# Kernel tuning notes

Hardware: AMD Instinct MI355X
Metric: run time of the kernel (lower is better)

## Reference

```python
import jax, jax.numpy as jnp
import numpy as np

N = 20000
E = 320000
IN_CH = 512
OUT_CH = 256


def setup_inputs() -> dict:
    key = jax.random.key(0)
    ks = jax.random.split(key, 24)
    p = lambda k, shape: jax.random.normal(k, shape, jnp.float32) * 0.05
    return {
        "x": jax.random.normal(ks[0], (N, IN_CH), jnp.float32),
        "edge_index": jax.random.randint(ks[1], (2, E), 0, N),
        "original_size": 16384,
        "W1": p(ks[2], (IN_CH, 4 * 256)), "as1": p(ks[3], (4, 256)), "ad1": p(ks[4], (4, 256)), "b1": p(ks[5], (1024,)),
        "lw1": p(ks[6], (IN_CH, 1024)), "lb1": p(ks[7], (1024,)),
        "W2": p(ks[8], (1024, 4 * 256)), "as2": p(ks[9], (4, 256)), "ad2": p(ks[10], (4, 256)), "b2": p(ks[11], (1024,)),
        "lw2": p(ks[12], (1024, 1024)), "lb2": p(ks[13], (1024,)),
        "W3": p(ks[14], (1024, 6 * 256)), "as3": p(ks[15], (6, 256)), "ad3": p(ks[16], (6, 256)), "b3": p(ks[17], (256,)),
        "lw3": p(ks[18], (1024, OUT_CH)), "lb3": p(ks[19], (OUT_CH,)),
    }


def gat_conv(x, src, dst, W, a_src, a_dst, bias, heads, ch, concat):
    """PyG-style GATConv: gather -> edge attention -> segment softmax -> scatter-add."""
    n = x.shape[0]
    h = (x @ W).reshape(n, heads, ch)                      # [N,H,C]
    alpha_s = (h * a_src[None]).sum(-1)                    # [N,H]
    alpha_d = (h * a_dst[None]).sum(-1)                    # [N,H]
    e = jax.nn.leaky_relu(alpha_s[src] + alpha_d[dst], 0.2)  # [E,H]
    m = jax.ops.segment_max(e, dst, num_segments=n)        # per-dst max (stable softmax)
    e = jnp.exp(e - m[dst])
    denom = jax.ops.segment_sum(e, dst, num_segments=n)
    alpha = e / (denom[dst] + 1e-16)                       # [E,H]
    msg = h[src] * alpha[:, :, None]                       # [E,H,C]
    out = jax.ops.segment_sum(msg, dst, num_segments=n)    # [N,H,C]
    out = out.reshape(n, heads * ch) if concat else out.mean(axis=1)
    return out + bias


def reference(x, edge_index, original_size, W1, as1, ad1, b1, lw1, lb1,
              W2, as2, ad2, b2, lw2, lb2, W3, as3, ad3, b3, lw3, lb3):
    n = x.shape[0]
    loops = jnp.arange(n)
    src = jnp.concatenate([edge_index[0], loops])  # PyG add_self_loops=True default
    dst = jnp.concatenate([edge_index[1], loops])
    h = jax.nn.elu(gat_conv(x, src, dst, W1, as1, ad1, b1, 4, 256, True) + x @ lw1 + lb1)
    h = jax.nn.elu(gat_conv(h, src, dst, W2, as2, ad2, b2, 4, 256, True) + h @ lw2 + lb2)
    h = gat_conv(h, src, dst, W3, as3, ad3, b3, 6, 256, False) + h @ lw3 + lb3
    return h[:original_size]
```

## Files before the change

### kernel.cpp

```cpp
#include <hip/hip_runtime.h>

#define N_NODES 20000
#define M_PAD   20096
#define E_EDGES 320000

typedef unsigned short u16;
typedef unsigned int   u32;
typedef __attribute__((ext_vector_type(8))) short bf16x8;
typedef __attribute__((ext_vector_type(4))) float f32x4;
typedef __attribute__((ext_vector_type(4))) u32   u32x4;

__device__ __forceinline__ float bf2f(u16 u){
  u32 x = ((u32)u) << 16; float f; __builtin_memcpy(&f, &x, 4); return f;
}
__device__ __forceinline__ u16 f2bf(float f){
  u32 u; __builtin_memcpy(&u, &f, 4);
  u += 0x7fffu + ((u >> 16) & 1u);
  return (u16)(u >> 16);
}

__device__ __forceinline__ void gl_lds16(const void* g, void* l){
  __builtin_amdgcn_global_load_lds((const __attribute__((address_space(1))) void*)g,
                                   (__attribute__((address_space(3))) void*)l, 16, 0, 0);
}

__device__ __forceinline__ void acc8(float* acc, float w, u32x4 p){
#pragma unroll
  for (int d = 0; d < 4; d++){
    u32 u = p[d];
    acc[2 * d]     += w * bf2f((u16)(u & 0xffff));
    acc[2 * d + 1] += w * bf2f((u16)(u >> 16));
  }
}

__global__ void hist_k(const int* __restrict__ ei, int* __restrict__ cnt){
  int i = blockIdx.x * 256 + threadIdx.x;
  if (i < E_EDGES) atomicAdd(&cnt[ei[E_EDGES + i]], 1);
}

__global__ void scan_k(const int* __restrict__ cnt, int* __restrict__ rowp,
                       int* __restrict__ fill, int n){
  __shared__ int wsum[16], wpre[16];
  __shared__ int carry;
  int tid = threadIdx.x, lane = tid & 63, wv = tid >> 6;
  if (tid == 0) carry = 0;
  __syncthreads();
  for (int base = 0; base < n; base += 1024){
    int i = base + tid;
    int v = (i < n) ? cnt[i] : 0;
    int incl = v;
#pragma unroll
    for (int d = 1; d < 64; d <<= 1){
      int t = __shfl_up(incl, d, 64);
      if (lane >= d) incl += t;
    }
    if (lane == 63) wsum[wv] = incl;
    __syncthreads();
    if (tid == 0){
      int s = carry;
#pragma unroll
      for (int w = 0; w < 16; w++){ wpre[w] = s; s += wsum[w]; }
      carry = s;
    }
    __syncthreads();
    if (i < n){ int e = wpre[wv] + incl - v; rowp[i] = e; fill[i] = e; }
  }
  __syncthreads();
  if (tid == 0) rowp[n] = carry;
}

__global__ void scatter_k(const int* __restrict__ ei, int* __restrict__ fill, int* __restrict__ esrc){
  int i = blockIdx.x * 256 + threadIdx.x;
  if (i < E_EDGES){
    int d = ei[E_EDGES + i];
    int p = atomicAdd(&fill[d], 1);
    esrc[p] = ei[i];
  }
}

__global__ void tcast_all(const float* __restrict__ W1, const float* __restrict__ lw1, u16* __restrict__ Wt1,
                          const float* __restrict__ W2, const float* __restrict__ lw2, u16* __restrict__ Wt2,
                          const float* __restrict__ W3, const float* __restrict__ lw3, u16* __restrict__ Wt3)
{
  __shared__ float tile[32][33];
  int b = blockIdx.x;
  const float* src; u16* dst; int Nc, n0, ldd;
  if      (b <  512){            src = W1;  Nc = 1024; dst = Wt1; n0 = 0;    ldd = 512;  }
  else if (b < 1024){ b -=  512; src = lw1; Nc = 1024; dst = Wt1; n0 = 1024; ldd = 512;  }
  else if (b < 2048){ b -= 1024; src = W2;  Nc = 1024; dst = Wt2; n0 = 0;    ldd = 1024; }
  else if (b < 3072){ b -= 2048; src = lw2; Nc = 1024; dst = Wt2; n0 = 1024; ldd = 1024; }
  else if (b < 4608){ b -= 3072; src = W3;  Nc = 1536; dst = Wt3; n0 = 0;    ldd = 1024; }
  else              { b -= 4608; src = lw3; Nc = 256;  dst = Wt3; n0 = 1536; ldd = 1024; }
  int gx = Nc / 32;
  int kb = (b / gx) * 32, nb = (b % gx) * 32;
  int tx = threadIdx.x, ty = threadIdx.y;
#pragma unroll
  for (int r = 0; r < 32; r += 8)
    tile[ty + r][tx] = src[(size_t)(kb + ty + r) * Nc + nb + tx];
  __syncthreads();
#pragma unroll
  for (int r = 0; r < 32; r += 8){
    int n = nb + ty + r;
    dst[(size_t)(n0 + n) * ldd + kb + tx] = f2bf(tile[tx][ty + r]);
  }
}

__global__ void castx_k(const float* __restrict__ x, u16* __restrict__ o, int realRows){
  int r = blockIdx.x, c = threadIdx.x * 2;
  float2 v = (r < realRows) ? *(const float2*)(x + (size_t)r * 512 + c) : make_float2(0.f, 0.f);
  u32 pk = ((u32)f2bf(v.y) << 16) | (u32)f2bf(v.x);
  *(u32*)(o + (size_t)r * 512 + c) = pk;
}

__global__ void zpad_k(u16* __restrict__ p, int n){
  int i = blockIdx.x * 256 + threadIdx.x; if (i < n) p[i] = 0;
}

__global__ __launch_bounds__(256, 2)
void gemm_bf16(const u16* __restrict__ A, const u16* __restrict__ Bt, u16* __restrict__ C,
               int N, int K,
               const float* __restrict__ a_s, const float* __restrict__ a_d,
               float* __restrict__ aS, float* __restrict__ aD, int H)
{
  __shared__ __attribute__((aligned(16))) u16 lA[128 * 32];
  __shared__ __attribute__((aligned(16))) u16 lB[256 * 32];
  const int tid  = threadIdx.x;
  const int wave = tid >> 6, lane = tid & 63;
  const int bn = blockIdx.x, bm = blockIdx.y;
  const int wm = (wave >> 1) * 64, wn = (wave & 1) * 128;

  const int srow  = wave * 16 + (lane >> 2);
  const int skcol = (lane & 3) * 8;
  const u16* Ag0 = A  + (size_t)(bm * 128 + srow) * K + skcol;
  const u16* Ag1 = Ag0 + (size_t)64 * K;
  const u16* Bg  = Bt + (size_t)(bn * 256 + srow) * K + skcol;
  u16* lA0 = lA + wave * 512; u16* lA1 = lA + 2048 + wave * 512;
  u16* lBw = lB + wave * 512;

  f32x4 acc[4][8] = {};

  for (int k0 = 0; k0 < K; k0 += 32){
    gl_lds16(Ag0 + k0, lA0);
    gl_lds16(Ag1 + k0, lA1);
#pragma unroll
    for (int c = 0; c < 4; c++)
      gl_lds16(Bg + (size_t)(c * 64) * K + k0, lBw + c * 2048);
    __syncthreads();
    const int koff = (lane >> 4) * 8;
    const int rsel = lane & 15;
    bf16x8 af[4], bfr[8];
#pragma unroll
    for (int i = 0; i < 4; i++) af[i]  = *(const bf16x8*)&lA[(wm + i * 16 + rsel) * 32 + koff];
#pragma unroll
    for (int j = 0; j < 8; j++) bfr[j] = *(const bf16x8*)&lB[(wn + j * 16 + rsel) * 32 + koff];
#pragma unroll
    for (int i = 0; i < 4; i++)
#pragma unroll
      for (int j = 0; j < 8; j++)
        acc[i][j] = __builtin_amdgcn_mfma_f32_16x16x32_bf16(af[i], bfr[j], acc[i][j], 0, 0, 0);
    __syncthreads();
  }

  const int r0 = (lane >> 4) * 4, cl = lane & 15;
#pragma unroll
  for (int i = 0; i < 4; i++)
#pragma unroll
    for (int j = 0; j < 8; j++){
      int row = bm * 128 + wm + i * 16 + r0;
      int col = bn * 256 + wn + j * 16 + cl;
      u16* cp = C + (size_t)row * N + col;
#pragma unroll
      for (int r = 0; r < 4; r++) cp[(size_t)r * N] = f2bf(acc[i][j][r]);
    }

  if (bn < H){
    float* fa = (float*)lA;
    fa[tid]       = a_s[bn * 256 + tid];
    fa[256 + tid] = a_d[bn * 256 + tid];
    __syncthreads();
    float* fb = (float*)lB;
    const int q = lane >> 4;
#pragma unroll
    for (int i = 0; i < 4; i++)
#pragma unroll
      for (int r = 0; r < 4; r++){
        float ps = 0.f, pd = 0.f;
#pragma unroll
        for (int j = 0; j < 8; j++){
          float v = acc[i][j][r];
          int c = wn + j * 16 + cl;
          ps += v * fa[c];
          pd += v * fa[256 + c];
        }
#pragma unroll
        for (int m = 1; m < 16; m <<= 1){
          ps += __shfl_xor(ps, m, 64);
          pd += __shfl_xor(pd, m, 64);
        }
        if (cl == 0){
          int row = wm + i * 16 + q * 4 + r;
          fb[(wave & 1) * 128 + row]       = ps;
          fb[256 + (wave & 1) * 128 + row] = pd;
        }
      }
    __syncthreads();
    if (tid < 128){
      int row = bm * 128 + tid;
      aS[(size_t)row * H + bn] = fb[tid] + fb[128 + tid];
      aD[(size_t)row * H + bn] = fb[256 + tid] + fb[384 + tid];
    }
  }
}

__global__ __launch_bounds__(256)
void agg4_k(const u16* __restrict__ HG, int ldH,
            const int* __restrict__ rowp, const int* __restrict__ esrc,
            const float* __restrict__ aS, const float* __restrict__ aD,
            const float* __restrict__ bias, const float* __restrict__ lbias,
            u16* __restrict__ outb)
{
  constexpr int MAXE = 320;
  __shared__ float s_m[4], s_dinv[4], s_red[16];
  __shared__ float s_ew[MAXE * 4];
  __shared__ int   s_src[MAXE];
  __shared__ float s_acc[2][1024];

  const int dst = blockIdx.x;
  const int tid = threadIdx.x, lane = tid & 63, wv = tid >> 6;
  const int e0 = rowp[dst];
  const int deg = rowp[dst + 1] - e0;
  const int nE = deg + 1;
  const bool fits = (nE <= MAXE);

  float4 adv = *(const float4*)(aD + (size_t)dst * 4);

  float lm[4] = { -1e30f, -1e30f, -1e30f, -1e30f };
  for (int i = tid; i < nE; i += 256){
    int s = (i == deg) ? dst : esrc[e0 + i];
    if (fits) s_src[i] = s;
    float4 as = *(const float4*)(aS + (size_t)s * 4);
    float e0h = as.x + adv.x; e0h = e0h > 0.f ? e0h : 0.2f * e0h;
    float e1h = as.y + adv.y; e1h = e1h > 0.f ? e1h : 0.2f * e1h;
    float e2h = as.z + adv.z; e2h = e2h > 0.f ? e2h : 0.2f * e2h;
    float e3h = as.w + adv.w; e3h = e3h > 0.f ? e3h : 0.2f * e3h;
    if (fits){ s_ew[i*4+0]=e0h; s_ew[i*4+1]=e1h; s_ew[i*4+2]=e2h; s_ew[i*4+3]=e3h; }
    lm[0] = fmaxf(lm[0], e0h); lm[1] = fmaxf(lm[1], e1h);
    lm[2] = fmaxf(lm[2], e2h); lm[3] = fmaxf(lm[3], e3h);
  }
#pragma unroll
  for (int h = 0; h < 4; h++)
#pragma unroll
    for (int off = 32; off; off >>= 1) lm[h] = fmaxf(lm[h], __shfl_down(lm[h], off));
  if (lane == 0){
#pragma unroll
    for (int h = 0; h < 4; h++) s_red[wv * 4 + h] = lm[h];
  }
  __syncthreads();
  if (tid < 4) s_m[tid] = fmaxf(fmaxf(s_red[tid], s_red[4 + tid]),
                                fmaxf(s_red[8 + tid], s_red[12 + tid]));
  __syncthreads();

  float ls[4] = {0.f, 0.f, 0.f, 0.f};
  for (int i = tid; i < nE; i += 256){
    if (fits){
#pragma unroll
      for (int h = 0; h < 4; h++){
        float w = __expf(s_ew[i * 4 + h] - s_m[h]);
        s_ew[i * 4 + h] = w;
        ls[h] += w;
      }
    } else {
      int s = (i == deg) ? dst : esrc[e0 + i];
      float4 as = *(const float4*)(aS + (size_t)s * 4);
      float e;
      e = as.x + adv.x; e = e > 0.f ? e : 0.2f * e; ls[0] += __expf(e - s_m[0]);
      e = as.y + adv.y; e = e > 0.f ? e : 0.2f * e; ls[1] += __expf(e - s_m[1]);
      e = as.z + adv.z; e = e > 0.f ? e : 0.2f * e; ls[2] += __expf(e - s_m[2]);
      e = as.w + adv.w; e = e > 0.f ? e : 0.2f * e; ls[3] += __expf(e - s_m[3]);
    }
  }
#pragma unroll
  for (int h = 0; h < 4; h++)
#pragma unroll
    for (int off = 32; off; off >>= 1) ls[h] += __shfl_down(ls[h], off);
  if (lane == 0){
#pragma unroll
    for (int h = 0; h < 4; h++) s_red[wv * 4 + h] = ls[h];
  }
  __syncthreads();
  if (tid < 4) s_dinv[tid] = 1.f / (s_red[tid] + s_red[4 + tid] + s_red[8 + tid] + s_red[12 + tid] + 1e-16f);
  __syncthreads();

  const int grp = wv >> 1;
  const int ch0 = (wv & 1) * 512 + lane * 8;
  const int h   = ch0 >> 8;
  const float dinv = s_dinv[h];
  const float mh   = s_m[h];
  float acc[8] = {};
  const u16* HGb = HG + ch0;

  if (fits){
    int i = grp;
    for (; i + 2 < nE; i += 4){
      int s0 = s_src[i], s1 = s_src[i + 2];
      float w0 = s_ew[i * 4 + h] * dinv;
      float w1 = s_ew[(i + 2) * 4 + h] * dinv;
      u32x4 p0 = *(const u32x4*)(HGb + (size_t)s0 * ldH);
      u32x4 p1 = *(const u32x4*)(HGb + (size_t)s1 * ldH);
      acc8(acc, w0, p0);
      acc8(acc, w1, p1);
    }
    if (i < nE){
      int s0 = s_src[i];
      float w0 = s_ew[i * 4 + h] * dinv;
      u32x4 p0 = *(const u32x4*)(HGb + (size_t)s0 * ldH);
      acc8(acc, w0, p0);
    }
  } else {
    float advh = aD[(size_t)dst * 4 + h];
    for (int i = grp; i < nE; i += 2){
      int s = (i == deg) ? dst : esrc[e0 + i];
      float e = aS[(size_t)s * 4 + h] + advh;
      e = e > 0.f ? e : 0.2f * e;
      float w = __expf(e - mh) * dinv;
      u32x4 p = *(const u32x4*)(HGb + (size_t)s * ldH);
      acc8(acc, w, p);
    }
  }
#pragma unroll
  for (int c = 0; c < 8; c++) s_acc[grp][ch0 + c] = acc[c];
  __syncthreads();

  const int c4 = tid * 4;
  const u16* lr = HG + (size_t)dst * ldH + 1024 + c4;
  ushort4 u = *(const ushort4*)lr;
  float lv[4] = { bf2f(u.x), bf2f(u.y), bf2f(u.z), bf2f(u.w) };
  ushort4 o;
  float v0 = s_acc[0][c4+0] + s_acc[1][c4+0] + bias[c4+0] + lv[0] + lbias[c4+0]; v0 = v0 > 0.f ? v0 : __expf(v0) - 1.f;
  float v1 = s_acc[0][c4+1] + s_acc[1][c4+1] + bias[c4+1] + lv[1] + lbias[c4+1]; v1 = v1 > 0.f ? v1 : __expf(v1) - 1.f;
  float v2 = s_acc[0][c4+2] + s_acc[1][c4+2] + bias[c4+2] + lv[2] + lbias[c4+2]; v2 = v2 > 0.f ? v2 : __expf(v2) - 1.f;
  float v3 = s_acc[0][c4+3] + s_acc[1][c4+3] + bias[c4+3] + lv[3] + lbias[c4+3]; v3 = v3 > 0.f ? v3 : __expf(v3) - 1.f;
  o.x = f2bf(v0); o.y = f2bf(v1); o.z = f2bf(v2); o.w = f2bf(v3);
  *(ushort4*)(outb + (size_t)dst * 1024 + c4) = o;
}

__global__ __launch_bounds__(384)
void agg6_k(const u16* __restrict__ HG, int ldH,
            const int* __restrict__ rowp, const int* __restrict__ esrc,
            const float* __restrict__ aS, const float* __restrict__ aD,
            const float* __restrict__ bias, const float* __restrict__ lbias,
            float* __restrict__ outf)
{
  constexpr int MAXE = 320;
  __shared__ float s_m[6], s_dinv[6], s_red[36];
  __shared__ float s_ew[MAXE * 6];
  __shared__ int   s_src[MAXE];
  __shared__ float s_acc[2][1536];

  const int dst = blockIdx.x;
  const int tid = threadIdx.x, lane = tid & 63, wv = tid >> 6;
  const int e0 = rowp[dst];
  const int deg = rowp[dst + 1] - e0;
  const int nE = deg + 1;
  const bool fits = (nE <= MAXE);

  float adv[6];
#pragma unroll
  for (int h = 0; h < 6; h++) adv[h] = aD[(size_t)dst * 6 + h];

  float lm[6];
#pragma unroll
  for (int h = 0; h < 6; h++) lm[h] = -1e30f;
  for (int i = tid; i < nE; i += 384){
    int s = (i == deg) ? dst : esrc[e0 + i];
    if (fits) s_src[i] = s;
#pragma unroll
    for (int h = 0; h < 6; h++){
      float e = aS[(size_t)s * 6 + h] + adv[h];
      e = e > 0.f ? e : 0.2f * e;
      if (fits) s_ew[i * 6 + h] = e;
      lm[h] = fmaxf(lm[h], e);
    }
  }
#pragma unroll
  for (int h = 0; h < 6; h++)
#pragma unroll
    for (int off = 32; off; off >>= 1) lm[h] = fmaxf(lm[h], __shfl_down(lm[h], off));
  if (lane == 0){
#pragma unroll
    for (int h = 0; h < 6; h++) s_red[wv * 6 + h] = lm[h];
  }
  __syncthreads();
  if (tid < 6){
    float m = s_red[tid];
#pragma unroll
    for (int w = 1; w < 6; w++) m = fmaxf(m, s_red[w * 6 + tid]);
    s_m[tid] = m;
  }
  __syncthreads();

  float ls[6];
#pragma unroll
  for (int h = 0; h < 6; h++) ls[h] = 0.f;
  for (int i = tid; i < nE; i += 384){
    if (fits){
#pragma unroll
      for (int h = 0; h < 6; h++){
        float w = __expf(s_ew[i * 6 + h] - s_m[h]);
        s_ew[i * 6 + h] = w;
        ls[h] += w;
      }
    } else {
      int s = (i == deg) ? dst : esrc[e0 + i];
#pragma unroll
      for (int h = 0; h < 6; h++){
        float e = aS[(size_t)s * 6 + h] + adv[h];
        e = e > 0.f ? e : 0.2f * e;
        ls[h] += __expf(e - s_m[h]);
      }
    }
  }
#pragma unroll
  for (int h = 0; h < 6; h++)
#pragma unroll
    for (int off = 32; off; off >>= 1) ls[h] += __shfl_down(ls[h], off);
  if (lane == 0){
#pragma unroll
    for (int h = 0; h < 6; h++) s_red[wv * 6 + h] = ls[h];
  }
  __syncthreads();
  if (tid < 6){
    float s = 0.f;
#pragma unroll
    for (int w = 0; w < 6; w++) s += s_red[w * 6 + tid];
    s_dinv[tid] = 1.f / (s + 1e-16f);
  }
  __syncthreads();

  const int grp  = wv / 3;
  const int wrow = wv - grp * 3;
  const int ch0  = wrow * 512 + lane * 8;
  const int h    = ch0 >> 8;
  const float dinv = s_dinv[h];
  const float mh   = s_m[h];
  float acc[8] = {};
  const u16* HGb = HG + ch0;

  if (fits){
    int i = grp;
    for (; i + 2 < nE; i += 4){
      int s0 = s_src[i], s1 = s_src[i + 2];
      float w0 = s_ew[i * 6 + h] * dinv;
      float w1 = s_ew[(i + 2) * 6 + h] * dinv;
      u32x4 p0 = *(const u32x4*)(HGb + (size_t)s0 * ldH);
      u32x4 p1 = *(const u32x4*)(HGb + (size_t)s1 * ldH);
      acc8(acc, w0, p0);
      acc8(acc, w1, p1);
    }
    if (i < nE){
      int s0 = s_src[i];
      float w0 = s_ew[i * 6 + h] * dinv;
      u32x4 p0 = *(const u32x4*)(HGb + (size_t)s0 * ldH);
      acc8(acc, w0, p0);
    }
  } else {
    float advh = aD[(size_t)dst * 6 + h];
    for (int i = grp; i < nE; i += 2){
      int s = (i == deg) ? dst : esrc[e0 + i];
      float e = aS[(size_t)s * 6 + h] + advh;
      e = e > 0.f ? e : 0.2f * e;
      float w = __expf(e - mh) * dinv;
      u32x4 p = *(const u32x4*)(HGb + (size_t)s * ldH);
      acc8(acc, w, p);
    }
  }
#pragma unroll
  for (int c = 0; c < 8; c++) s_acc[grp][ch0 + c] = acc[c];
  __syncthreads();

  if (tid < 256){
    int c = tid;
    float v = 0.f;
#pragma unroll
    for (int hh = 0; hh < 6; hh++) v += s_acc[0][hh * 256 + c] + s_acc[1][hh * 256 + c];
    v = v * (1.f / 6.f) + bias[c] + bf2f(HG[(size_t)dst * ldH + 1536 + c]) + lbias[c];
    outf[(size_t)dst * 256 + c] = v;
  }
}

extern "C" void kernel_launch(void* const* d_in, const int* in_sizes, int n_in,
                              void* d_out, int out_size, void* d_ws, size_t ws_size,
                              hipStream_t stream)
{
  const float* x   = (const float*)d_in[0];
  const int*   ei  = (const int*)  d_in[1];
  const float* W1  = (const float*)d_in[3];
  const float* as1 = (const float*)d_in[4];
  const float* ad1 = (const float*)d_in[5];
  const float* b1  = (const float*)d_in[6];
  const float* lw1 = (const float*)d_in[7];
  const float* lb1 = (const float*)d_in[8];
  const float* W2  = (const float*)d_in[9];
  const float* as2 = (const float*)d_in[10];
  const float* ad2 = (const float*)d_in[11];
  const float* b2  = (const float*)d_in[12];
  const float* lw2 = (const float*)d_in[13];
  const float* lb2 = (const float*)d_in[14];
  const float* W3  = (const float*)d_in[15];
  const float* as3 = (const float*)d_in[16];
  const float* ad3 = (const float*)d_in[17];
  const float* b3  = (const float*)d_in[18];
  const float* lw3 = (const float*)d_in[19];
  const float* lb3 = (const float*)d_in[20];

  char* wp = (char*)d_ws;
  auto nxt = [&](size_t b) -> void* {
    void* p = (void*)wp; wp += (b + 255) & ~(size_t)255; return p;
  };
  u16*  Wt1  = (u16*) nxt((size_t)2048 * 512  * 2);
  u16*  Wt2  = (u16*) nxt((size_t)2048 * 1024 * 2);
  u16*  Wt3  = (u16*) nxt((size_t)1792 * 1024 * 2);
  u16*  Xb   = (u16*) nxt((size_t)M_PAD * 1024 * 2);
  u16*  HG   = (u16*) nxt((size_t)M_PAD * 2048 * 2);
  float* aS  = (float*)nxt((size_t)M_PAD * 6 * 4);
  float* aD  = (float*)nxt((size_t)M_PAD * 6 * 4);
  int*  cnt  = (int*)  nxt((size_t)N_NODES * 4);
  int*  rowp = (int*)  nxt((size_t)(N_NODES + 1) * 4);
  int*  fill = (int*)  nxt((size_t)N_NODES * 4);
  int*  esrc = (int*)  nxt((size_t)E_EDGES * 4);

  hipMemsetAsync(cnt, 0, (size_t)N_NODES * 4, stream);
  hist_k   <<<(E_EDGES + 255) / 256, 256, 0, stream>>>(ei, cnt);
  scan_k   <<<1, 1024, 0, stream>>>(cnt, rowp, fill, N_NODES);
  scatter_k<<<(E_EDGES + 255) / 256, 256, 0, stream>>>(ei, fill, esrc);

  tcast_all<<<4864, dim3(32, 8), 0, stream>>>(W1, lw1, Wt1, W2, lw2, Wt2, W3, lw3, Wt3);

  castx_k<<<M_PAD, 256, 0, stream>>>(x, Xb, N_NODES);
  zpad_k <<<(96 * 1024 + 255) / 256, 256, 0, stream>>>(Xb + (size_t)N_NODES * 1024, 96 * 1024);

  const int MT = M_PAD / 128;

  gemm_bf16<<<dim3(2048 / 256, MT), 256, 0, stream>>>(Xb, Wt1, HG, 2048, 512,  as1, ad1, aS, aD, 4);
  agg4_k   <<<N_NODES, 256, 0, stream>>>(HG, 2048, rowp, esrc, aS, aD, b1, lb1, Xb);

  gemm_bf16<<<dim3(2048 / 256, MT), 256, 0, stream>>>(Xb, Wt2, HG, 2048, 1024, as2, ad2, aS, aD, 4);
  agg4_k   <<<N_NODES, 256, 0, stream>>>(HG, 2048, rowp, esrc, aS, aD, b2, lb2, Xb);

  gemm_bf16<<<dim3(1792 / 256, MT), 256, 0, stream>>>(Xb, Wt3, HG, 1792, 1024, as3, ad3, aS, aD, 6);
  int outRows = out_size / 256;
  agg6_k   <<<outRows, 384, 0, stream>>>(HG, 1792, rowp, esrc, aS, aD, b3, lb3, (float*)d_out);

  (void)in_sizes; (void)n_in; (void)ws_size;
}
```

Before: 873.7 us.

## Aggregate one destination node per wavefront instead of one per block

The GAT aggregation kernels now give each 64-lane wavefront a whole destination node, four nodes per block. Softmax max and sum use wave shuffles instead of block-wide shared-memory reductions and several barriers. Each lane holds one edge's source and weight, so the first 64 edges are broadcast by shuffle, and each lane accumulates 16 or 24 channels. The per-node attention-score arrays are padded to a stride of 8 so they can be read with vector loads. Degrees above 64 fall back to a serial loop that recomputes the weights, and the launch grid assumes the node count divides by 4.

After: 865.2 us. Within noise of the previous version (-1.0%).

```diff
diff --git a/kernel.cpp b/kernel.cpp
--- a/kernel.cpp
+++ b/kernel.cpp
@@ -18,6 +18,7 @@
   u += 0x7fffu + ((u >> 16) & 1u);
   return (u16)(u >> 16);
 }
+__device__ __forceinline__ float lrelu(float x){ return x > 0.f ? x : 0.2f * x; }
 
 __device__ __forceinline__ void gl_lds16(const void* g, void* l){
   __builtin_amdgcn_global_load_lds((const __attribute__((address_space(1))) void*)g,
@@ -31,6 +32,25 @@
     acc[2 * d]     += w * bf2f((u16)(u & 0xffff));
     acc[2 * d + 1] += w * bf2f((u16)(u >> 16));
   }
+}
+
+__device__ __forceinline__ void acc24(float* acc, float w0, float w1, int bnd,
+                                      u32x4 p0, u32x4 p1, u32x4 p2){
+  u32 u[12];
+  *(u32x4*)(u) = p0; *(u32x4*)(u + 4) = p1; *(u32x4*)(u + 8) = p2;
+#pragma unroll
+  for (int d = 0; d < 12; d++){
+    float w = (2 * d < bnd) ? w0 : w1;
+    acc[2 * d]     += w * bf2f((u16)(u[d] & 0xffff));
+    acc[2 * d + 1] += w * bf2f((u16)(u[d] >> 16));
+  }
+}
+
+__device__ __forceinline__ float sel6(const float* a, int h){
+  float r = a[0];
+  r = (h == 1) ? a[1] : r; r = (h == 2) ? a[2] : r; r = (h == 3) ? a[3] : r;
+  r = (h == 4) ? a[4] : r; r = (h == 5) ? a[5] : r;
+  return r;
 }
 
 __global__ void hist_k(const int* __restrict__ ei, int* __restrict__ cnt){
@@ -206,286 +226,238 @@
     __syncthreads();
     if (tid < 128){
       int row = bm * 128 + tid;
-      aS[(size_t)row * H + bn] = fb[tid] + fb[128 + tid];
-      aD[(size_t)row * H + bn] = fb[256 + tid] + fb[384 + tid];
+      aS[(size_t)row * 8 + bn] = fb[tid] + fb[128 + tid];
+      aD[(size_t)row * 8 + bn] = fb[256 + tid] + fb[384 + tid];
     }
   }
 }
 
 __global__ __launch_bounds__(256)
-void agg4_k(const u16* __restrict__ HG, int ldH,
-            const int* __restrict__ rowp, const int* __restrict__ esrc,
-            const float* __restrict__ aS, const float* __restrict__ aD,
-            const float* __restrict__ bias, const float* __restrict__ lbias,
-            u16* __restrict__ outb)
+void agg4w_k(const u16* __restrict__ HG, int ldH,
+             const int* __restrict__ rowp, const int* __restrict__ esrc,
+             const float* __restrict__ aS, const float* __restrict__ aD,
+             const float* __restrict__ bias, const float* __restrict__ lbias,
+             u16* __restrict__ outb)
 {
-  constexpr int MAXE = 320;
-  __shared__ float s_m[4], s_dinv[4], s_red[16];
-  __shared__ float s_ew[MAXE * 4];
-  __shared__ int   s_src[MAXE];
-  __shared__ float s_acc[2][1024];
-
-  const int dst = blockIdx.x;
+  __shared__ float s_w[4][256];
   const int tid = threadIdx.x, lane = tid & 63, wv = tid >> 6;
+  const int dst = blockIdx.x * 4 + wv;
   const int e0 = rowp[dst];
   const int deg = rowp[dst + 1] - e0;
   const int nE = deg + 1;
-  const bool fits = (nE <= MAXE);
-
-  float4 adv = *(const float4*)(aD + (size_t)dst * 4);
-
-  float lm[4] = { -1e30f, -1e30f, -1e30f, -1e30f };
-  for (int i = tid; i < nE; i += 256){
+  const float4 adv = *(const float4*)(aD + (size_t)dst * 8);
+
+  int myS = dst;
+  float ea = -1e30f, eb = -1e30f, ec = -1e30f, ed = -1e30f;
+  if (lane < nE){
+    myS = (lane == deg) ? dst : esrc[e0 + lane];
+    float4 as = *(const float4*)(aS + (size_t)myS * 8);
+    ea = lrelu(as.x + adv.x); eb = lrelu(as.y + adv.y);
+    ec = lrelu(as.z + adv.z); ed = lrelu(as.w + adv.w);
+  }
+  float m0 = ea, m1 = eb, m2 = ec, m3 = ed;
+  for (int i = lane + 64; i < nE; i += 64){
     int s = (i == deg) ? dst : esrc[e0 + i];
-    if (fits) s_src[i] = s;
-    float4 as = *(const float4*)(aS + (size_t)s * 4);
-    float e0h = as.x + adv.x; e0h = e0h > 0.f ? e0h : 0.2f * e0h;
-    float e1h = as.y + adv.y; e1h = e1h > 0.f ? e1h : 0.2f * e1h;
-    float e2h = as.z + adv.z; e2h = e2h > 0.f ? e2h : 0.2f * e2h;
-    float e3h = as.w + adv.w; e3h = e3h > 0.f ? e3h : 0.2f * e3h;
-    if (fits){ s_ew[i*4+0]=e0h; s_ew[i*4+1]=e1h; s_ew[i*4+2]=e2h; s_ew[i*4+3]=e3h; }
-    lm[0] = fmaxf(lm[0], e0h); lm[1] = fmaxf(lm[1], e1h);
-    lm[2] = fmaxf(lm[2], e2h); lm[3] = fmaxf(lm[3], e3h);
-  }
-#pragma unroll
-  for (int h = 0; h < 4; h++)
-#pragma unroll
-    for (int off = 32; off; off >>= 1) lm[h] = fmaxf(lm[h], __shfl_down(lm[h], off));
-  if (lane == 0){
-#pragma unroll
-    for (int h = 0; h < 4; h++) s_red[wv * 4 + h] = lm[h];
-  }
+    float4 as = *(const float4*)(aS + (size_t)s * 8);
+    m0 = fmaxf(m0, lrelu(as.x + adv.x)); m1 = fmaxf(m1, lrelu(as.y + adv.y));
+    m2 = fmaxf(m2, lrelu(as.z + adv.z)); m3 = fmaxf(m3, lrelu(as.w + adv.w));
+  }
+#pragma unroll
+  for (int off = 1; off < 64; off <<= 1){
+    m0 = fmaxf(m0, __shfl_xor(m0, off)); m1 = fmaxf(m1, __shfl_xor(m1, off));
+    m2 = fmaxf(m2, __shfl_xor(m2, off)); m3 = fmaxf(m3, __shfl_xor(m3, off));
+  }
+
+  float w0 = __expf(ea - m0), w1 = __expf(eb - m1);
+  float w2 = __expf(ec - m2), w3 = __expf(ed - m3);
+  float l0 = w0, l1 = w1, l2 = w2, l3 = w3;
+  for (int i = lane + 64; i < nE; i += 64){
+    int s = (i == deg) ? dst : esrc[e0 + i];
+    float4 as = *(const float4*)(aS + (size_t)s * 8);
+    l0 += __expf(lrelu(as.x + adv.x) - m0); l1 += __expf(lrelu(as.y + adv.y) - m1);
+    l2 += __expf(lrelu(as.z + adv.z) - m2); l3 += __expf(lrelu(as.w + adv.w) - m3);
+  }
+#pragma unroll
+  for (int off = 1; off < 64; off <<= 1){
+    l0 += __shfl_xor(l0, off); l1 += __shfl_xor(l1, off);
+    l2 += __shfl_xor(l2, off); l3 += __shfl_xor(l3, off);
+  }
+  float d0 = 1.f / (l0 + 1e-16f), d1 = 1.f / (l1 + 1e-16f);
+  float d2 = 1.f / (l2 + 1e-16f), d3 = 1.f / (l3 + 1e-16f);
+  *(float4*)&s_w[wv][lane * 4] = make_float4(w0 * d0, w1 * d1, w2 * d2, w3 * d3);
   __syncthreads();
-  if (tid < 4) s_m[tid] = fmaxf(fmaxf(s_red[tid], s_red[4 + tid]),
-                                fmaxf(s_red[8 + tid], s_red[12 + tid]));
-  __syncthreads();
-
-  float ls[4] = {0.f, 0.f, 0.f, 0.f};
-  for (int i = tid; i < nE; i += 256){
-    if (fits){
-#pragma unroll
-      for (int h = 0; h < 4; h++){
-        float w = __expf(s_ew[i * 4 + h] - s_m[h]);
-        s_ew[i * 4 + h] = w;
-        ls[h] += w;
-      }
-    } else {
-      int s = (i == deg) ? dst : esrc[e0 + i];
-      float4 as = *(const float4*)(aS + (size_t)s * 4);
-      float e;
-      e = as.x + adv.x; e = e > 0.f ? e : 0.2f * e; ls[0] += __expf(e - s_m[0]);
-      e = as.y + adv.y; e = e > 0.f ? e : 0.2f * e; ls[1] += __expf(e - s_m[1]);
-      e = as.z + adv.z; e = e > 0.f ? e : 0.2f * e; ls[2] += __expf(e - s_m[2]);
-      e = as.w + adv.w; e = e > 0.f ? e : 0.2f * e; ls[3] += __expf(e - s_m[3]);
-    }
-  }
-#pragma unroll
-  for (int h = 0; h < 4; h++)
-#pragma unroll
-    for (int off = 32; off; off >>= 1) ls[h] += __shfl_down(ls[h], off);
-  if (lane == 0){
-#pragma unroll
-    for (int h = 0; h < 4; h++) s_red[wv * 4 + h] = ls[h];
-  }
-  __syncthreads();
-  if (tid < 4) s_dinv[tid] = 1.f / (s_red[tid] + s_red[4 + tid] + s_red[8 + tid] + s_red[12 + tid] + 1e-16f);
-  __syncthreads();
-
-  const int grp = wv >> 1;
-  const int ch0 = (wv & 1) * 512 + lane * 8;
-  const int h   = ch0 >> 8;
-  const float dinv = s_dinv[h];
-  const float mh   = s_m[h];
-  float acc[8] = {};
-  const u16* HGb = HG + ch0;
-
-  if (fits){
-    int i = grp;
-    for (; i + 2 < nE; i += 4){
-      int s0 = s_src[i], s1 = s_src[i + 2];
-      float w0 = s_ew[i * 4 + h] * dinv;
-      float w1 = s_ew[(i + 2) * 4 + h] * dinv;
-      u32x4 p0 = *(const u32x4*)(HGb + (size_t)s0 * ldH);
-      u32x4 p1 = *(const u32x4*)(HGb + (size_t)s1 * ldH);
-      acc8(acc, w0, p0);
-      acc8(acc, w1, p1);
-    }
-    if (i < nE){
-      int s0 = s_src[i];
-      float w0 = s_ew[i * 4 + h] * dinv;
-      u32x4 p0 = *(const u32x4*)(HGb + (size_t)s0 * ldH);
-      acc8(acc, w0, p0);
-    }
-  } else {
-    float advh = aD[(size_t)dst * 4 + h];
-    for (int i = grp; i < nE; i += 2){
-      int s = (i == deg) ? dst : esrc[e0 + i];
-      float e = aS[(size_t)s * 4 + h] + advh;
-      e = e > 0.f ? e : 0.2f * e;
-      float w = __expf(e - mh) * dinv;
-      u32x4 p = *(const u32x4*)(HGb + (size_t)s * ldH);
-      acc8(acc, w, p);
-    }
-  }
-#pragma unroll
-  for (int c = 0; c < 8; c++) s_acc[grp][ch0 + c] = acc[c];
-  __syncthreads();
-
-  const int c4 = tid * 4;
-  const u16* lr = HG + (size_t)dst * ldH + 1024 + c4;
-  ushort4 u = *(const ushort4*)lr;
-  float lv[4] = { bf2f(u.x), bf2f(u.y), bf2f(u.z), bf2f(u.w) };
-  ushort4 o;
-  float v0 = s_acc[0][c4+0] + s_acc[1][c4+0] + bias[c4+0] + lv[0] + lbias[c4+0]; v0 = v0 > 0.f ? v0 : __expf(v0) - 1.f;
-  float v1 = s_acc[0][c4+1] + s_acc[1][c4+1] + bias[c4+1] + lv[1] + lbias[c4+1]; v1 = v1 > 0.f ? v1 : __expf(v1) - 1.f;
-  float v2 = s_acc[0][c4+2] + s_acc[1][c4+2] + bias[c4+2] + lv[2] + lbias[c4+2]; v2 = v2 > 0.f ? v2 : __expf(v2) - 1.f;
-  float v3 = s_acc[0][c4+3] + s_acc[1][c4+3] + bias[c4+3] + lv[3] + lbias[c4+3]; v3 = v3 > 0.f ? v3 : __expf(v3) - 1.f;
-  o.x = f2bf(v0); o.y = f2bf(v1); o.z = f2bf(v2); o.w = f2bf(v3);
-  *(ushort4*)(outb + (size_t)dst * 1024 + c4) = o;
-}
-
-__global__ __launch_bounds__(384)
-void agg6_k(const u16* __restrict__ HG, int ldH,
-            const int* __restrict__ rowp, const int* __restrict__ esrc,
-            const float* __restrict__ aS, const float* __restrict__ aD,
-            const float* __restrict__ bias, const float* __restrict__ lbias,
-            float* __restrict__ outf)
+
+  const int h = lane >> 4;
+  const int ch0 = lane * 16;
+  const float mh   = (h < 2) ? (h == 0 ? m0 : m1) : (h == 2 ? m2 : m3);
+  const float dh   = (h < 2) ? (h == 0 ? d0 : d1) : (h == 2 ? d2 : d3);
+  const float advh = (h < 2) ? (h == 0 ? adv.x : adv.y) : (h == 2 ? adv.z : adv.w);
+  float acc[16] = {};
+  const u16* HGc = HG + ch0;
+  const int nF = nE < 64 ? nE : 64;
+  int i = 0;
+  for (; i + 1 < nF; i += 2){
+    int sA = __shfl(myS, i), sB = __shfl(myS, i + 1);
+    float wA = s_w[wv][i * 4 + h], wB = s_w[wv][(i + 1) * 4 + h];
+    const u16* ra = HGc + (size_t)sA * ldH;
+    const u16* rb = HGc + (size_t)sB * ldH;
+    u32x4 pa0 = *(const u32x4*)ra, pa1 = *(const u32x4*)(ra + 8);
+    u32x4 pb0 = *(const u32x4*)rb, pb1 = *(const u32x4*)(rb + 8);
+    acc8(acc, wA, pa0); acc8(acc + 8, wA, pa1);
+    acc8(acc, wB, pb0); acc8(acc + 8, wB, pb1);
+  }
+  if (i < nF){
+    int sA = __shfl(myS, i);
+    float wA = s_w[wv][i * 4 + h];
+    const u16* ra = HGc + (size_t)sA * ldH;
+    acc8(acc, wA, *(const u32x4*)ra); acc8(acc + 8, wA, *(const u32x4*)(ra + 8));
+  }
+  for (int j = 64; j < nE; j++){
+    int s = (j == deg) ? dst : esrc[e0 + j];
+    float e = lrelu(aS[(size_t)s * 8 + h] + advh);
+    float w = __expf(e - mh) * dh;
+    const u16* r = HGc + (size_t)s * ldH;
+    acc8(acc, w, *(const u32x4*)r); acc8(acc + 8, w, *(const u32x4*)(r + 8));
+  }
+
+  const u16* lr = HG + (size_t)dst * ldH + 1024 + ch0;
+  u32x4 q0 = *(const u32x4*)lr, q1 = *(const u32x4*)(lr + 8);
+  float lin[16];
+#pragma unroll
+  for (int d = 0; d < 4; d++){
+    lin[2*d]     = bf2f((u16)(q0[d] & 0xffff)); lin[2*d+1]   = bf2f((u16)(q0[d] >> 16));
+    lin[8+2*d]   = bf2f((u16)(q1[d] & 0xffff)); lin[8+2*d+1] = bf2f((u16)(q1[d] >> 16));
+  }
+  u32 o[8];
+#pragma unroll
+  for (int d = 0; d < 8; d++){
+    float va = acc[2*d]   + bias[ch0 + 2*d]   + lin[2*d]   + lbias[ch0 + 2*d];
+    float vb = acc[2*d+1] + bias[ch0 + 2*d+1] + lin[2*d+1] + lbias[ch0 + 2*d+1];
+    va = va > 0.f ? va : __expf(va) - 1.f;
+    vb = vb > 0.f ? vb : __expf(vb) - 1.f;
+    o[d] = ((u32)f2bf(vb) << 16) | (u32)f2bf(va);
+  }
+  u16* op = outb + (size_t)dst * 1024 + ch0;
+  *(u32x4*)op = *(u32x4*)o;
+  *(u32x4*)(op + 8) = *(u32x4*)(o + 4);
+}
+
+__global__ __launch_bounds__(256)
+void agg6w_k(const u16* __restrict__ HG, int ldH,
+             const int* __restrict__ rowp, const int* __restrict__ esrc,
+             const float* __restrict__ aS, const float* __restrict__ aD,
+             const float* __restrict__ bias, const float* __restrict__ lbias,
+             float* __restrict__ outf)
 {
-  constexpr int MAXE = 320;
-  __shared__ float s_m[6], s_dinv[6], s_red[36];
-  __shared__ float s_ew[MAXE * 6];
-  __shared__ int   s_src[MAXE];
-  __shared__ float s_acc[2][1536];
-
-  const int dst = blockIdx.x;
+  __shared__ float s_w[4][64 * 6];
+  __shared__ float s_fin[4][1536];
   const int tid = threadIdx.x, lane = tid & 63, wv = tid >> 6;
+  const int dst = blockIdx.x * 4 + wv;
   const int e0 = rowp[dst];
   const int deg = rowp[dst + 1] - e0;
   const int nE = deg + 1;
-  const bool fits = (nE <= MAXE);
-
-  float adv[6];
-#pragma unroll
-  for (int h = 0; h < 6; h++) adv[h] = aD[(size_t)dst * 6 + h];
-
-  float lm[6];
-#pragma unroll
-  for (int h = 0; h < 6; h++) lm[h] = -1e30f;
-  for (int i = tid; i < nE; i += 384){
+
+  const float* advp = aD + (size_t)dst * 8;
+  float4 av4 = *(const float4*)advp; float2 av2 = *(const float2*)(advp + 4);
+  float adv[6] = { av4.x, av4.y, av4.z, av4.w, av2.x, av2.y };
+
+  int myS = dst;
+  float e[6];
+#pragma unroll
+  for (int h = 0; h < 6; h++) e[h] = -1e30f;
+  if (lane < nE){
+    myS = (lane == deg) ? dst : esrc[e0 + lane];
+    float4 a0 = *(const float4*)(aS + (size_t)myS * 8);
+    float2 a1 = *(const float2*)(aS + (size_t)myS * 8 + 4);
+    e[0] = lrelu(a0.x + adv[0]); e[1] = lrelu(a0.y + adv[1]);
+    e[2] = lrelu(a0.z + adv[2]); e[3] = lrelu(a0.w + adv[3]);
+    e[4] = lrelu(a1.x + adv[4]); e[5] = lrelu(a1.y + adv[5]);
+  }
+  float m[6];
+#pragma unroll
+  for (int h = 0; h < 6; h++) m[h] = e[h];
+  for (int i = lane + 64; i < nE; i += 64){
     int s = (i == deg) ? dst : esrc[e0 + i];
-    if (fits) s_src[i] = s;
-#pragma unroll
-    for (int h = 0; h < 6; h++){
-      float e = aS[(size_t)s * 6 + h] + adv[h];
-      e = e > 0.f ? e : 0.2f * e;
-      if (fits) s_ew[i * 6 + h] = e;
-      lm[h] = fmaxf(lm[h], e);
-    }
+    float4 a0 = *(const float4*)(aS + (size_t)s * 8);
+    float2 a1 = *(const float2*)(aS + (size_t)s * 8 + 4);
+    float t[6] = { a0.x, a0.y, a0.z, a0.w, a1.x, a1.y };
+#pragma unroll
+    for (int h = 0; h < 6; h++) m[h] = fmaxf(m[h], lrelu(t[h] + adv[h]));
   }
 #pragma unroll
   for (int h = 0; h < 6; h++)
 #pragma unroll
-    for (int off = 32; off; off >>= 1) lm[h] = fmaxf(lm[h], __shfl_down(lm[h], off));
-  if (lane == 0){
-#pragma unroll
-    for (int h = 0; h < 6; h++) s_red[wv * 6 + h] = lm[h];
-  }
+    for (int off = 1; off < 64; off <<= 1) m[h] = fmaxf(m[h], __shfl_xor(m[h], off));
+
+  float w[6], l[6];
+#pragma unroll
+  for (int h = 0; h < 6; h++){ w[h] = __expf(e[h] - m[h]); l[h] = w[h]; }
+  for (int i = lane + 64; i < nE; i += 64){
+    int s = (i == deg) ? dst : esrc[e0 + i];
+    float4 a0 = *(const float4*)(aS + (size_t)s * 8);
+    float2 a1 = *(const float2*)(aS + (size_t)s * 8 + 4);
+    float t[6] = { a0.x, a0.y, a0.z, a0.w, a1.x, a1.y };
+#pragma unroll
+    for (int h = 0; h < 6; h++) l[h] += __expf(lrelu(t[h] + adv[h]) - m[h]);
+  }
+#pragma unroll
+  for (int h = 0; h < 6; h++)
+#pragma unroll
+    for (int off = 1; off < 64; off <<= 1) l[h] += __shfl_xor(l[h], off);
+  float dv[6];
+#pragma unroll
+  for (int h = 0; h < 6; h++) dv[h] = 1.f / (l[h] + 1e-16f);
+  float* swp = &s_w[wv][lane * 6];
+  ((float2*)swp)[0] = make_float2(w[0] * dv[0], w[1] * dv[1]);
+  ((float2*)swp)[1] = make_float2(w[2] * dv[2], w[3] * dv[3]);
+  ((float2*)swp)[2] = make_float2(w[4] * dv[4], w[5] * dv[5]);
   __syncthreads();
-  if (tid < 6){
-    float m = s_red[tid];
-#pragma unroll
-    for (int w = 1; w < 6; w++) m = fmaxf(m, s_red[w * 6 + tid]);
-    s_m[tid] = m;
-  }
+
+  const int ch0 = lane * 24;
+  const int h0 = ch0 >> 8, h1 = (ch0 + 23) >> 8;
+  const int bnd = (h0 + 1) * 256 - ch0;
+  const float mh0 = sel6(m, h0), mh1 = sel6(m, h1);
+  const float dh0 = sel6(dv, h0), dh1 = sel6(dv, h1);
+  const float ah0 = sel6(adv, h0), ah1 = sel6(adv, h1);
+  float acc[24] = {};
+  const u16* HGc = HG + ch0;
+  const int nF = nE < 64 ? nE : 64;
+  for (int i = 0; i < nF; i++){
+    int s = __shfl(myS, i);
+    float wA0 = s_w[wv][i * 6 + h0], wA1 = s_w[wv][i * 6 + h1];
+    const u16* r = HGc + (size_t)s * ldH;
+    acc24(acc, wA0, wA1, bnd,
+          *(const u32x4*)r, *(const u32x4*)(r + 8), *(const u32x4*)(r + 16));
+  }
+  for (int j = 64; j < nE; j++){
+    int s = (j == deg) ? dst : esrc[e0 + j];
+    float w0 = __expf(lrelu(aS[(size_t)s * 8 + h0] + ah0) - mh0) * dh0;
+    float w1 = __expf(lrelu(aS[(size_t)s * 8 + h1] + ah1) - mh1) * dh1;
+    const u16* r = HGc + (size_t)s * ldH;
+    acc24(acc, w0, w1, bnd,
+          *(const u32x4*)r, *(const u32x4*)(r + 8), *(const u32x4*)(r + 16));
+  }
+#pragma unroll
+  for (int d = 0; d < 6; d++)
+    *(float4*)&s_fin[wv][ch0 + d * 4] = make_float4(acc[4*d], acc[4*d+1], acc[4*d+2], acc[4*d+3]);
   __syncthreads();
 
-  float ls[6];
-#pragma unroll
-  for (int h = 0; h < 6; h++) ls[h] = 0.f;
-  for (int i = tid; i < nE; i += 384){
-    if (fits){
-#pragma unroll
-      for (int h = 0; h < 6; h++){
-        float w = __expf(s_ew[i * 6 + h] - s_m[h]);
-        s_ew[i * 6 + h] = w;
-        ls[h] += w;
-      }
-    } else {
-      int s = (i == deg) ? dst : esrc[e0 + i];
-#pragma unroll
-      for (int h = 0; h < 6; h++){
-        float e = aS[(size_t)s * 6 + h] + adv[h];
-        e = e > 0.f ? e : 0.2f * e;
-        ls[h] += __expf(e - s_m[h]);
-      }
-    }
-  }
-#pragma unroll
-  for (int h = 0; h < 6; h++)
-#pragma unroll
-    for (int off = 32; off; off >>= 1) ls[h] += __shfl_down(ls[h], off);
-  if (lane == 0){
-#pragma unroll
-    for (int h = 0; h < 6; h++) s_red[wv * 6 + h] = ls[h];
-  }
-  __syncthreads();
-  if (tid < 6){
-    float s = 0.f;
-#pragma unroll
-    for (int w = 0; w < 6; w++) s += s_red[w * 6 + tid];
-    s_dinv[tid] = 1.f / (s + 1e-16f);
-  }
-  __syncthreads();
-
-  const int grp  = wv / 3;
-  const int wrow = wv - grp * 3;
-  const int ch0  = wrow * 512 + lane * 8;
-  const int h    = ch0 >> 8;
-  const float dinv = s_dinv[h];
-  const float mh   = s_m[h];
-  float acc[8] = {};
-  const u16* HGb = HG + ch0;
-
-  if (fits){
-    int i = grp;
-    for (; i + 2 < nE; i += 4){
-      int s0 = s_src[i], s1 = s_src[i + 2];
-      float w0 = s_ew[i * 6 + h] * dinv;
-      float w1 = s_ew[(i + 2) * 6 + h] * dinv;
-      u32x4 p0 = *(const u32x4*)(HGb + (size_t)s0 * ldH);
-      u32x4 p1 = *(const u32x4*)(HGb + (size_t)s1 * ldH);
-      acc8(acc, w0, p0);
-      acc8(acc, w1, p1);
-    }
-    if (i < nE){
-      int s0 = s_src[i];
-      float w0 = s_ew[i * 6 + h] * dinv;
-      u32x4 p0 = *(const u32x4*)(HGb + (size_t)s0 * ldH);
-      acc8(acc, w0, p0);
-    }
-  } else {
-    float advh = aD[(size_t)dst * 6 + h];
-    for (int i = grp; i < nE; i += 2){
-      int s = (i == deg) ? dst : esrc[e0 + i];
-      float e = aS[(size_t)s * 6 + h] + advh;
-      e = e > 0.f ? e : 0.2f * e;
-      float w = __expf(e - mh) * dinv;
-      u32x4 p = *(const u32x4*)(HGb + (size_t)s * ldH);
-      acc8(acc, w, p);
-    }
-  }
-#pragma unroll
-  for (int c = 0; c < 8; c++) s_acc[grp][ch0 + c] = acc[c];
-  __syncthreads();
-
-  if (tid < 256){
-    int c = tid;
-    float v = 0.f;
-#pragma unroll
-    for (int hh = 0; hh < 6; hh++) v += s_acc[0][hh * 256 + c] + s_acc[1][hh * 256 + c];
-    v = v * (1.f / 6.f) + bias[c] + bf2f(HG[(size_t)dst * ldH + 1536 + c]) + lbias[c];
-    outf[(size_t)dst * 256 + c] = v;
-  }
+  const int c0 = lane * 4;
+  float4 sum = make_float4(0.f, 0.f, 0.f, 0.f);
+#pragma unroll
+  for (int h = 0; h < 6; h++){
+    float4 t = *(const float4*)&s_fin[wv][h * 256 + c0];
+    sum.x += t.x; sum.y += t.y; sum.z += t.z; sum.w += t.w;
+  }
+  ushort4 uq = *(const ushort4*)(HG + (size_t)dst * ldH + 1536 + c0);
+  float4 bv = *(const float4*)(bias + c0);
+  float4 lb = *(const float4*)(lbias + c0);
+  float4 o;
+  o.x = sum.x * (1.f/6.f) + bv.x + bf2f(uq.x) + lb.x;
+  o.y = sum.y * (1.f/6.f) + bv.y + bf2f(uq.y) + lb.y;
+  o.z = sum.z * (1.f/6.f) + bv.z + bf2f(uq.z) + lb.z;
+  o.w = sum.w * (1.f/6.f) + bv.w + bf2f(uq.w) + lb.w;
+  *(float4*)(outf + (size_t)dst * 256 + c0) = o;
 }
 
 extern "C" void kernel_launch(void* const* d_in, const int* in_sizes, int n_in,
@@ -504,8 +476,8 @@
   const float* as2 = (const float*)d_in[10];
   const float* ad2 = (const float*)d_in[11];
   const float* b2  = (const float*)d_in[12];
+  const float* lb2p= (const float*)d_in[14];
   const float* lw2 = (const float*)d_in[13];
-  const float* lb2 = (const float*)d_in[14];
   const float* W3  = (const float*)d_in[15];
   const float* as3 = (const float*)d_in[16];
   const float* ad3 = (const float*)d_in[17];
@@ -522,8 +494,8 @@
   u16*  Wt3  = (u16*) nxt((size_t)1792 * 1024 * 2);
   u16*  Xb   = (u16*) nxt((size_t)M_PAD * 1024 * 2);
   u16*  HG   = (u16*) nxt((size_t)M_PAD * 2048 * 2);
-  float* aS  = (float*)nxt((size_t)M_PAD * 6 * 4);
-  float* aD  = (float*)nxt((size_t)M_PAD * 6 * 4);
+  float* aS  = (float*)nxt((size_t)M_PAD * 8 * 4);
+  float* aD  = (float*)nxt((size_t)M_PAD * 8 * 4);
   int*  cnt  = (int*)  nxt((size_t)N_NODES * 4);
   int*  rowp = (int*)  nxt((size_t)(N_NODES + 1) * 4);
   int*  fill = (int*)  nxt((size_t)N_NODES * 4);
@@ -542,14 +514,14 @@
   const int MT = M_PAD / 128;
 
   gemm_bf16<<<dim3(2048 / 256, MT), 256, 0, stream>>>(Xb, Wt1, HG, 2048, 512,  as1, ad1, aS, aD, 4);
-  agg4_k   <<<N_NODES, 256, 0, stream>>>(HG, 2048, rowp, esrc, aS, aD, b1, lb1, Xb);
+  agg4w_k  <<<N_NODES / 4, 256, 0, stream>>>(HG, 2048, rowp, esrc, aS, aD, b1, lb1, Xb);
 
   gemm_bf16<<<dim3(2048 / 256, MT), 256, 0, stream>>>(Xb, Wt2, HG, 2048, 1024, as2, ad2, aS, aD, 4);
-  agg4_k   <<<N_NODES, 256, 0, stream>>>(HG, 2048, rowp, esrc, aS, aD, b2, lb2, Xb);
+  agg4w_k  <<<N_NODES / 4, 256, 0, stream>>>(HG, 2048, rowp, esrc, aS, aD, b2, lb2p, Xb);
 
   gemm_bf16<<<dim3(1792 / 256, MT), 256, 0, stream>>>(Xb, Wt3, HG, 1792, 1024, as3, ad3, aS, aD, 6);
   int outRows = out_size / 256;
-  agg6_k   <<<outRows, 384, 0, stream>>>(HG, 1792, rowp, esrc, aS, aD, b3, lb3, (float*)d_out);
+  agg6w_k  <<<outRows / 4, 256, 0, stream>>>(HG, 1792, rowp, esrc, aS, aD, b3, lb3, (float*)d_out);
 
   (void)in_sizes; (void)n_in; (void)ws_size;
 }
```
